# Performance work log

Hardware: AMD Instinct MI355X
Metric: run time of the kernel (lower is better)

The kernel has to match this reference:

```python
import jax, jax.numpy as jnp
import numpy as np

D = 256      # d_model
L = 2        # num_layers
N = 10000    # num_nodes
E = 160000   # num_edges (avg degree 16)
EPS = 1e-5


def _ln(h, g, b):
    m = jnp.mean(h, axis=-1, keepdims=True)
    v = jnp.mean(jnp.square(h - m), axis=-1, keepdims=True)
    return (h - m) / jnp.sqrt(v + EPS) * g + b


def _lrelu(h):
    return jnp.where(h > 0, h, 0.2 * h)


def setup_inputs() -> dict:
    key = jax.random.key(0)
    ks = jax.random.split(key, 24)
    p = lambda k, shape: (jax.random.normal(k, shape, dtype=jnp.float32) * 0.05)
    inp = {
        "edge_index": jax.random.randint(ks[0], (2, E), 0, N),
        "x": jax.random.normal(ks[1], (N, D), dtype=jnp.float32),
        # per-layer attention / FF params (torch Linear convention: W is [out, in])
        "Wq": p(ks[2], (L, D, D)), "bq": p(ks[3], (L, D)),
        "Wk": p(ks[4], (L, D, D)), "bk": p(ks[5], (L, D)),
        "Wv": p(ks[6], (L, D, D)), "bv": p(ks[7], (L, D)),
        "Wff": p(ks[8], (L, D, D)), "bff": p(ks[9], (L, D)),
        # LayerNorm params
        "ga": jnp.ones((L, D), jnp.float32), "ba": jnp.zeros((L, D), jnp.float32),
        "gf": jnp.ones((L, D), jnp.float32), "bf": jnp.zeros((L, D), jnp.float32),
        "gfin": jnp.ones((D,), jnp.float32), "bfin": jnp.zeros((D,), jnp.float32),
        # head MLP
        "W3": p(ks[10], (3 * D, D)), "b3": p(ks[11], (3 * D,)),
        "W4": p(ks[12], (3 * D, 3 * D)), "b4": p(ks[13], (3 * D,)),
        "W5": p(ks[14], (D, 3 * D)), "b5": p(ks[15], (D,)),
        "Wvec": p(ks[16], (1, D)), "bvec": p(ks[17], (1,)),
    }
    return inp


def reference(edge_index, x, Wq, bq, Wk, bk, Wv, bv, Wff, bff,
              ga, ba, gf, bf, gfin, bfin, W3, b3, W4, b4, W5, b5, Wvec, bvec):
    num_nodes = x.shape[0]
    src = edge_index[0]  # [E]
    dst = edge_index[1]  # [E] (segment-softmax target)
    x_i = x[src]         # [E, D]
    query = x[dst]       # [E, D] (x_j)
    for i in range(Wq.shape[0]):
        q = query @ Wq[i].T + bq[i]            # [E, D]
        k = x_i @ Wk[i].T + bk[i]
        v = x_i @ Wv[i].T + bv[i]
        alpha = jnp.sum(q * k, axis=-1)        # [E]
        # segment softmax over dst
        amax = jax.ops.segment_max(alpha, dst, num_segments=num_nodes)
        e = jnp.exp(alpha - amax[dst])
        denom = jax.ops.segment_sum(e, dst, num_segments=num_nodes)
        attn = e / denom[dst]                  # [E]
        attn_out = q + attn[:, None] * v       # [E, D]
        query = _ln(attn_out, ga[i], ba[i])
        query = query @ Wff[i].T + bff[i]
    query = _lrelu(query)
    query = _ln(query, gf[0], bf[0])           # dropout = identity (eval)
    h = _lrelu(query @ W3.T + b3)              # [E, 3D]
    h = _lrelu(h @ W4.T + b4)                  # [E, 3D]
    h = h @ W5.T + b5                          # [E, D]
    h = _ln(h + query, gfin, bfin)
    adj_logits = (h @ Wvec.T + bvec)[:, 0]     # [E]
    return adj_logits
```

## Files before the change

### kernel.cpp

```cpp
#include <hip/hip_runtime.h>

#define D 256

typedef unsigned short u16;
typedef unsigned int u32;
typedef __attribute__((ext_vector_type(8))) short short8;
typedef __attribute__((ext_vector_type(4))) float f32x4;
typedef __attribute__((ext_vector_type(16))) float f32x16;

__device__ __forceinline__ float b2f(u16 u) {
    return __uint_as_float(((u32)u) << 16);
}
__device__ __forceinline__ u16 f2b(float f) {
    u32 u = __float_as_uint(f);
    return (u16)((u + 0x7FFFu + ((u >> 16) & 1u)) >> 16);
}
__device__ __forceinline__ u32 packf(float v) {
    u16 h = f2b(v);
    u16 l = f2b(v - b2f(h));
    return ((u32)h << 16) | l;
}
__device__ __forceinline__ float unpackf(u32 p) {
    return b2f((u16)(p >> 16)) + b2f((u16)(p & 0xffffu));
}
template<typename T> __device__ __forceinline__ float ld1(const T* p);
template<> __device__ __forceinline__ float ld1<u16>(const u16* p) { return b2f(*p); }
template<> __device__ __forceinline__ float ld1<u32>(const u32* p) { return unpackf(*p); }

__device__ __forceinline__ u32 f2ord(float f) {
    u32 b = __float_as_uint(f);
    return (b & 0x80000000u) ? ~b : (b | 0x80000000u);
}
__device__ __forceinline__ float ord2f(u32 u) {
    return (u & 0x80000000u) ? __uint_as_float(u & 0x7fffffffu)
                             : __uint_as_float(~u);
}

__device__ __forceinline__ float wred(float v) {
#pragma unroll
    for (int m = 32; m; m >>= 1) v += __shfl_xor(v, m);
    return v;
}

__device__ __forceinline__ void gl_lds16(const u16* g, u16* l) {
    __builtin_amdgcn_global_load_lds(
        (__attribute__((address_space(1))) void*)(u16*)g,
        (__attribute__((address_space(3))) void*)l, 16, 0, 0);
}

#define VMCNT(n) asm volatile("s_waitcnt vmcnt(" #n ")" ::: "memory")

template<int ACT>
__global__ __launch_bounds__(512, 1)
void gemm2(const u16* __restrict__ A, const u16* __restrict__ Whi,
           const float* __restrict__ bias, u16* __restrict__ C,
           int M, int N, int K)
{
    __shared__ u16 sA[2][128 * 64];
    __shared__ u16 sWh[2][256 * 64];

    const int tid  = threadIdx.x;
    const int lane = tid & 63;
    const int w    = tid >> 6;
    const int wm   = (w & 1) * 64;
    const int wn   = (w >> 1) * 64;
    const int row0 = blockIdx.x * 128;
    const int col0 = blockIdx.y * 256;

    f32x16 acc[2][2];
#pragma unroll
    for (int i = 0; i < 2; ++i)
#pragma unroll
        for (int j = 0; j < 2; ++j)
#pragma unroll
            for (int r = 0; r < 16; ++r) acc[i][j][r] = 0.f;

    const int r31   = lane & 31;
    const int khalf = lane >> 5;
    const int skey  = (r31 & 7) ^ ((r31 >> 3) & 3);
    const int l8r = lane >> 3;
    const int l8c = lane & 7;

    auto STAGE = [&](int b, int k0) {
#pragma unroll
        for (int s = 0; s < 4; ++s) {
            const int rbase = w * 32 + s * 8;
            const int row = rbase + l8r;
            const int gch = l8c ^ (row & 7) ^ s;
            gl_lds16(Whi + (size_t)(col0 + row) * K + k0 + gch * 8,
                     &sWh[b][rbase * 64]);
        }
#pragma unroll
        for (int s = 0; s < 2; ++s) {
            const int rbase = w * 16 + s * 8;
            const int row = rbase + l8r;
            const int gch = l8c ^ (row & 7) ^ ((w * 2 + s) & 3);
            gl_lds16(A + (size_t)(row0 + row) * K + k0 + gch * 8,
                     &sA[b][rbase * 64]);
        }
    };

    auto COMPUTE = [&](int b) {
#pragma unroll
        for (int w4 = 0; w4 < 4; ++w4) {
            const int slot = ((w4 * 2 + khalf) ^ skey) * 8;
            short8 af[2], wf[2];
#pragma unroll
            for (int i = 0; i < 2; ++i)
                af[i] = *(const short8*)(&sA[b][(wm + i * 32 + r31) * 64 + slot]);
#pragma unroll
            for (int j = 0; j < 2; ++j)
                wf[j] = *(const short8*)(&sWh[b][(wn + j * 32 + r31) * 64 + slot]);
#pragma unroll
            for (int i = 0; i < 2; ++i)
#pragma unroll
                for (int j = 0; j < 2; ++j)
                    acc[i][j] = __builtin_amdgcn_mfma_f32_32x32x16_bf16(af[i], wf[j], acc[i][j], 0, 0, 0);
        }
    };

    const int nt = K >> 6;
    STAGE(0, 0);
    STAGE(1, 64);
    int cur = 0;
    for (int t = 0; t < nt - 1; ++t) {
        VMCNT(6);
        __builtin_amdgcn_s_barrier();
        COMPUTE(cur);
        __builtin_amdgcn_s_barrier();
        if (t + 2 < nt) STAGE(cur, (t + 2) << 6);
        cur ^= 1;
    }
    VMCNT(0);
    __builtin_amdgcn_s_barrier();
    COMPUTE(cur);

#pragma unroll
    for (int j = 0; j < 2; ++j) {
        const int col = col0 + wn + j * 32 + r31;
        const float bb = bias[col];
#pragma unroll
        for (int i = 0; i < 2; ++i) {
            const int rowb = row0 + wm + i * 32 + 4 * khalf;
#pragma unroll
            for (int reg = 0; reg < 16; ++reg) {
                const int row = rowb + (reg & 3) + 8 * (reg >> 2);
                float v = acc[i][j][reg] + bb;
                if (ACT) v = v > 0.f ? v : 0.2f * v;
                C[(size_t)row * N + col] = f2b(v);
            }
        }
    }
}

__global__ __launch_bounds__(512, 4)
void gemm3w(const u32* __restrict__ Ap,
            const u16* __restrict__ Whi, const u16* __restrict__ Wlo,
            const float* __restrict__ bias,
            u32* __restrict__ Cp, u16* __restrict__ Chi,
            int M, int K, int act)
{
    constexpr int N = 256;
    __shared__ u16 sAhi[128 * 32];
    __shared__ u16 sAlo[128 * 32];
    __shared__ u16 sWhi[256 * 32];
    __shared__ u16 sWlo[256 * 32];

    const int tid  = threadIdx.x;
    const int lane = tid & 63;
    const int w    = tid >> 6;
    const int wm   = (w & 1) * 64;
    const int wn   = (w >> 1) * 64;
    const int row0 = blockIdx.x * 128;

    f32x4 acc[4][4];
#pragma unroll
    for (int i = 0; i < 4; ++i)
#pragma unroll
        for (int j = 0; j < 4; ++j) acc[i][j] = (f32x4){0.f, 0.f, 0.f, 0.f};

    const int lrow = lane >> 2;
    const int gck  = (lane & 3) ^ ((lane >> 3) & 3);
    const int r15 = lane & 15;
    const int rck = ((lane >> 4) ^ ((r15 >> 1) & 3)) * 8;

    for (int k0 = 0; k0 < K; k0 += 32) {
#pragma unroll
        for (int s = 0; s < 2; ++s) {
            const int rbase = w * 32 + s * 16;
            const size_t gW = (size_t)(rbase + lrow) * K + k0 + gck * 8;
            gl_lds16(Whi + gW, sWhi + rbase * 32);
            gl_lds16(Wlo + gW, sWlo + rbase * 32);
        }
#pragma unroll
        for (int it = 0; it < 2; ++it) {
            const int u = tid + it * 512;
            const int ar = u >> 3;
            const int pos = u & 7;
            uint4 pk = *(const uint4*)(Ap + (size_t)(row0 + ar) * K + k0 + pos * 4);
            const int slot = (pos >> 1) ^ ((ar >> 1) & 3);
            const int base = ar * 32 + slot * 8 + (pos & 1) * 4;
            ushort4 h4, l4;
            h4.x = (u16)(pk.x >> 16); l4.x = (u16)(pk.x & 0xffffu);
            h4.y = (u16)(pk.y >> 16); l4.y = (u16)(pk.y & 0xffffu);
            h4.z = (u16)(pk.z >> 16); l4.z = (u16)(pk.z & 0xffffu);
            h4.w = (u16)(pk.w >> 16); l4.w = (u16)(pk.w & 0xffffu);
            *(ushort4*)(sAhi + base) = h4;
            *(ushort4*)(sAlo + base) = l4;
        }
        __syncthreads();

        short8 ah[4], al[4], wh[4], wl[4];
#pragma unroll
        for (int i = 0; i < 4; ++i) {
            const int offA = (wm + i * 16 + r15) * 32 + rck;
            ah[i] = *(const short8*)(sAhi + offA);
            al[i] = *(const short8*)(sAlo + offA);
        }
#pragma unroll
        for (int j = 0; j < 4; ++j) {
            const int offW = (wn + j * 16 + r15) * 32 + rck;
            wh[j] = *(const short8*)(sWhi + offW);
            wl[j] = *(const short8*)(sWlo + offW);
        }
#pragma unroll
        for (int i = 0; i < 4; ++i)
#pragma unroll
            for (int j = 0; j < 4; ++j) {
                acc[i][j] = __builtin_amdgcn_mfma_f32_16x16x32_bf16(ah[i], wh[j], acc[i][j], 0, 0, 0);
                acc[i][j] = __builtin_amdgcn_mfma_f32_16x16x32_bf16(ah[i], wl[j], acc[i][j], 0, 0, 0);
                acc[i][j] = __builtin_amdgcn_mfma_f32_16x16x32_bf16(al[i], wh[j], acc[i][j], 0, 0, 0);
            }
        __syncthreads();
    }

#pragma unroll
    for (int j = 0; j < 4; ++j) {
        const int col = wn + j * 16 + r15;
        const float bb = bias[col];
#pragma unroll
        for (int i = 0; i < 4; ++i) {
            const int rowb = row0 + wm + i * 16 + (lane >> 4) * 4;
#pragma unroll
            for (int r = 0; r < 4; ++r) {
                float v = acc[i][j][r] + bb;
                if (act) v = v > 0.f ? v : 0.2f * v;
                const size_t idx = (size_t)(rowb + r) * N + col;
                if (Cp) Cp[idx] = packf(v);
                else    Chi[idx] = f2b(v);
            }
        }
    }
}

__global__ __launch_bounds__(512, 4)
void gemm3n(const u32* __restrict__ Ap,
            const u16* __restrict__ Whi, const u16* __restrict__ Wlo,
            const float* __restrict__ b0, const float* __restrict__ b1,
            const float* __restrict__ b2,
            u32* __restrict__ Cp, int M, int K)
{
    constexpr int N = 256;
    __shared__ u16 sAhi[128 * 32];
    __shared__ u16 sAlo[128 * 32];
    __shared__ u16 sWhi[256 * 32];
    __shared__ u16 sWlo[256 * 32];

    const int tid  = threadIdx.x;
    const int lane = tid & 63;
    const int w    = tid >> 6;
    const int wm   = (w & 1) * 64;
    const int wn   = (w >> 1) * 64;
    const int row0 = blockIdx.x * 128;
    const int y    = blockIdx.y;
    const float* bias = (y == 0) ? b0 : ((y == 1) ? b1 : b2);
    const u16* Wh = Whi + (size_t)y * N * K;
    const u16* Wl = Wlo + (size_t)y * N * K;
    u32* Cy = Cp + (size_t)y * M * N;

    f32x4 acc[4][4];
#pragma unroll
    for (int i = 0; i < 4; ++i)
#pragma unroll
        for (int j = 0; j < 4; ++j) acc[i][j] = (f32x4){0.f, 0.f, 0.f, 0.f};

    const int lrow = lane >> 2;
    const int gck  = (lane & 3) ^ ((lane >> 3) & 3);
    const int r15 = lane & 15;
    const int rck = ((lane >> 4) ^ ((r15 >> 1) & 3)) * 8;

    for (int k0 = 0; k0 < K; k0 += 32) {
#pragma unroll
        for (int s = 0; s < 2; ++s) {
            const int rbase = w * 32 + s * 16;
            const size_t gW = (size_t)(rbase + lrow) * K + k0 + gck * 8;
            gl_lds16(Wh + gW, sWhi + rbase * 32);
            gl_lds16(Wl + gW, sWlo + rbase * 32);
        }
#pragma unroll
        for (int it = 0; it < 2; ++it) {
            const int u = tid + it * 512;
            const int ar = u >> 3;
            const int pos = u & 7;
            int arc = row0 + ar; if (arc >= M) arc = M - 1;
            uint4 pk = *(const uint4*)(Ap + (size_t)arc * K + k0 + pos * 4);
            const int slot = (pos >> 1) ^ ((ar >> 1) & 3);
            const int base = ar * 32 + slot * 8 + (pos & 1) * 4;
            ushort4 h4, l4;
            h4.x = (u16)(pk.x >> 16); l4.x = (u16)(pk.x & 0xffffu);
            h4.y = (u16)(pk.y >> 16); l4.y = (u16)(pk.y & 0xffffu);
            h4.z = (u16)(pk.z >> 16); l4.z = (u16)(pk.z & 0xffffu);
            h4.w = (u16)(pk.w >> 16); l4.w = (u16)(pk.w & 0xffffu);
            *(ushort4*)(sAhi + base) = h4;
            *(ushort4*)(sAlo + base) = l4;
        }
        __syncthreads();

        short8 ah[4], al[4], wh[4], wl[4];
#pragma unroll
        for (int i = 0; i < 4; ++i) {
            const int offA = (wm + i * 16 + r15) * 32 + rck;
            ah[i] = *(const short8*)(sAhi + offA);
            al[i] = *(const short8*)(sAlo + offA);
        }
#pragma unroll
        for (int j = 0; j < 4; ++j) {
            const int offW = (wn + j * 16 + r15) * 32 + rck;
            wh[j] = *(const short8*)(sWhi + offW);
            wl[j] = *(const short8*)(sWlo + offW);
        }
#pragma unroll
        for (int i = 0; i < 4; ++i)
#pragma unroll
            for (int j = 0; j < 4; ++j) {
                acc[i][j] = __builtin_amdgcn_mfma_f32_16x16x32_bf16(ah[i], wh[j], acc[i][j], 0, 0, 0);
                acc[i][j] = __builtin_amdgcn_mfma_f32_16x16x32_bf16(ah[i], wl[j], acc[i][j], 0, 0, 0);
                acc[i][j] = __builtin_amdgcn_mfma_f32_16x16x32_bf16(al[i], wh[j], acc[i][j], 0, 0, 0);
            }
        __syncthreads();
    }

#pragma unroll
    for (int j = 0; j < 4; ++j) {
        const int col = wn + j * 16 + r15;
        const float bb = bias[col];
#pragma unroll
        for (int i = 0; i < 4; ++i) {
            const int rowb = row0 + wm + i * 16 + (lane >> 4) * 4;
#pragma unroll
            for (int r = 0; r < 4; ++r) {
                const int row = rowb + r;
                if (row < M)
                    Cy[(size_t)row * N + col] = packf(acc[i][j][r] + bb);
            }
        }
    }
}

__global__ void pack_x(const float* __restrict__ x, u32* __restrict__ xp, int n)
{
    int i = blockIdx.x * 256 + threadIdx.x;
    if (i < n) xp[i] = packf(x[i]);
}

__global__ void wconv(const float* __restrict__ wsrc, u16* __restrict__ hi,
                      u16* __restrict__ lo, int n)
{
    int i = blockIdx.x * 256 + threadIdx.x;
    if (i < n) {
        float v = wsrc[i];
        u16 h = f2b(v);
        hi[i] = h;
        if (lo) lo[i] = f2b(v - b2f(h));
    }
}

__global__ void seg_init(u32* __restrict__ amax, float* __restrict__ denom, int n)
{
    int i = blockIdx.x * 256 + threadIdx.x;
    if (i < n) { amax[i] = 0u; denom[i] = 0.f; }
}

template<typename TQ, int MODE>
__global__ __launch_bounds__(256)
void attn_alpha(const int* __restrict__ src, const int* __restrict__ dst,
                const TQ* __restrict__ qn, const u32* __restrict__ kn,
                float* __restrict__ alpha, u32* __restrict__ amax, int E)
{
    int e = blockIdx.x * 4 + (threadIdx.x >> 6);
    int lane = threadIdx.x & 63;
    if (e >= E) return;
    int s = src[e], d = dst[e];
    const TQ* qp = MODE ? (qn + (size_t)e * D) : (qn + (size_t)d * D);
    const u32* kp = kn + (size_t)s * D;
    float dot = 0.f;
#pragma unroll
    for (int j = 0; j < 4; ++j)
        dot += ld1(qp + lane * 4 + j) * unpackf(kp[lane * 4 + j]);
    dot = wred(dot);
    if (lane == 0) {
        alpha[e] = dot;
        atomicMax(amax + d, f2ord(dot));
    }
}

__global__ void seg_exp(const int* __restrict__ dst, const float* __restrict__ alpha,
                        const u32* __restrict__ amax, float* __restrict__ ebuf,
                        float* __restrict__ denom, int E)
{
    int e = blockIdx.x * 256 + threadIdx.x;
    if (e >= E) return;
    int d = dst[e];
    float ex = expf(alpha[e] - ord2f(amax[d]));
    ebuf[e] = ex;
    atomicAdd(denom + d, ex);
}

template<typename TQ, int MODE>
__global__ __launch_bounds__(256)
void attn_out_ln(const int* __restrict__ src, const int* __restrict__ dst,
                 const TQ* __restrict__ qn, const u32* __restrict__ vn,
                 const float* __restrict__ ebuf, const float* __restrict__ denom,
                 const float* __restrict__ g, const float* __restrict__ bb,
                 u32* __restrict__ outp, int e0, int cm)
{
    int le = blockIdx.x * 4 + (threadIdx.x >> 6);
    int lane = threadIdx.x & 63;
    if (le >= cm) return;
    int ge = e0 + le;
    int s = src[ge], d = dst[ge];
    float attn = ebuf[ge] / denom[d];
    const TQ* qp = MODE ? (qn + (size_t)ge * D) : (qn + (size_t)d * D);
    const u32* vp = vn + (size_t)s * D;
    int d0 = lane * 4;
    float a0 = ld1(qp + d0 + 0) + attn * unpackf(vp[d0 + 0]);
    float a1 = ld1(qp + d0 + 1) + attn * unpackf(vp[d0 + 1]);
    float a2 = ld1(qp + d0 + 2) + attn * unpackf(vp[d0 + 2]);
    float a3 = ld1(qp + d0 + 3) + attn * unpackf(vp[d0 + 3]);
    float mean = wred(a0 + a1 + a2 + a3) * (1.f / D);
    float c0 = a0 - mean, c1 = a1 - mean, c2 = a2 - mean, c3 = a3 - mean;
    float var = wred(c0 * c0 + c1 * c1 + c2 * c2 + c3 * c3) * (1.f / D);
    float rstd = rsqrtf(var + 1e-5f);
    uint4 p;
    p.x = packf(c0 * rstd * g[d0 + 0] + bb[d0 + 0]);
    p.y = packf(c1 * rstd * g[d0 + 1] + bb[d0 + 1]);
    p.z = packf(c2 * rstd * g[d0 + 2] + bb[d0 + 2]);
    p.w = packf(c3 * rstd * g[d0 + 3] + bb[d0 + 3]);
    *(uint4*)(outp + (size_t)le * D + d0) = p;
}

__global__ __launch_bounds__(256)
void lrelu_ln(const u32* __restrict__ inp, const float* __restrict__ g,
              const float* __restrict__ bb, u16* __restrict__ out, int cm)
{
    int le = blockIdx.x * 4 + (threadIdx.x >> 6);
    int lane = threadIdx.x & 63;
    if (le >= cm) return;
    size_t base = (size_t)le * D + lane * 4;
    uint4 xp = *(const uint4*)(inp + base);
    float x0 = unpackf(xp.x), x1 = unpackf(xp.y);
    float x2 = unpackf(xp.z), x3 = unpackf(xp.w);
    float a0 = x0 > 0.f ? x0 : 0.2f * x0;
    float a1 = x1 > 0.f ? x1 : 0.2f * x1;
    float a2 = x2 > 0.f ? x2 : 0.2f * x2;
    float a3 = x3 > 0.f ? x3 : 0.2f * x3;
    float mean = wred(a0 + a1 + a2 + a3) * (1.f / D);
    float c0 = a0 - mean, c1 = a1 - mean, c2 = a2 - mean, c3 = a3 - mean;
    float var = wred(c0 * c0 + c1 * c1 + c2 * c2 + c3 * c3) * (1.f / D);
    float rstd = rsqrtf(var + 1e-5f);
    int d0 = lane * 4;
    ushort4 o;
    o.x = f2b(c0 * rstd * g[d0 + 0] + bb[d0 + 0]);
    o.y = f2b(c1 * rstd * g[d0 + 1] + bb[d0 + 1]);
    o.z = f2b(c2 * rstd * g[d0 + 2] + bb[d0 + 2]);
    o.w = f2b(c3 * rstd * g[d0 + 3] + bb[d0 + 3]);
    *(ushort4*)(out + base) = o;
}

__global__ __launch_bounds__(256)
void final_k(const u16* __restrict__ hp, const u16* __restrict__ qp,
             const float* __restrict__ gfin, const float* __restrict__ bfin,
             const float* __restrict__ wvec, const float* __restrict__ bvec,
             float* __restrict__ out, int e0, int cm)
{
    int le = blockIdx.x * 4 + (threadIdx.x >> 6);
    int lane = threadIdx.x & 63;
    if (le >= cm) return;
    size_t base = (size_t)le * D + lane * 4;
    ushort4 hv = *(const ushort4*)(hp + base);
    ushort4 qv = *(const ushort4*)(qp + base);
    float a0 = b2f(hv.x) + b2f(qv.x);
    float a1 = b2f(hv.y) + b2f(qv.y);
    float a2 = b2f(hv.z) + b2f(qv.z);
    float a3 = b2f(hv.w) + b2f(qv.w);
    float mean = wred(a0 + a1 + a2 + a3) * (1.f / D);
    float c0 = a0 - mean, c1 = a1 - mean, c2 = a2 - mean, c3 = a3 - mean;
    float var = wred(c0 * c0 + c1 * c1 + c2 * c2 + c3 * c3) * (1.f / D);
    float rstd = rsqrtf(var + 1e-5f);
    int d0 = lane * 4;
    float t0 = c0 * rstd * gfin[d0 + 0] + bfin[d0 + 0];
    float t1 = c1 * rstd * gfin[d0 + 1] + bfin[d0 + 1];
    float t2 = c2 * rstd * gfin[d0 + 2] + bfin[d0 + 2];
    float t3 = c3 * rstd * gfin[d0 + 3] + bfin[d0 + 3];
    float part = t0 * wvec[d0 + 0] + t1 * wvec[d0 + 1] +
                 t2 * wvec[d0 + 2] + t3 * wvec[d0 + 3];
    part = wred(part);
    if (lane == 0) out[e0 + le] = part + bvec[0];
}

extern "C" void kernel_launch(void* const* d_in, const int* in_sizes, int n_in,
                              void* d_out, int out_size, void* d_ws, size_t ws_size,
                              hipStream_t stream)
{
    const int*   ei   = (const int*)d_in[0];
    const float* x    = (const float*)d_in[1];
    const float* Wq   = (const float*)d_in[2];
    const float* bq   = (const float*)d_in[3];
    const float* Wk   = (const float*)d_in[4];
    const float* bk   = (const float*)d_in[5];
    const float* Wv   = (const float*)d_in[6];
    const float* bv   = (const float*)d_in[7];
    const float* Wff  = (const float*)d_in[8];
    const float* bff  = (const float*)d_in[9];
    const float* ga   = (const float*)d_in[10];
    const float* ba   = (const float*)d_in[11];
    const float* gf   = (const float*)d_in[12];
    const float* bf   = (const float*)d_in[13];
    const float* gfin = (const float*)d_in[14];
    const float* bfin = (const float*)d_in[15];
    const float* W3   = (const float*)d_in[16];
    const float* b3   = (const float*)d_in[17];
    const float* W4   = (const float*)d_in[18];
    const float* b4   = (const float*)d_in[19];
    const float* W5   = (const float*)d_in[20];
    const float* b5   = (const float*)d_in[21];
    const float* Wvec = (const float*)d_in[22];
    const float* bvec = (const float*)d_in[23];

    const int E  = in_sizes[0] / 2;
    const int Nn = in_sizes[1] / D;
    const int* src = ei;
    const int* dst = ei + E;

    char* base = (char*)d_ws;
    size_t off = 0;
    auto take = [&](size_t bytes) -> void* {
        off = (off + 255) & ~(size_t)255;
        void* r = base + off;
        off += bytes;
        return r;
    };
    u32*   nKV1 = (u32*)take((size_t)2 * Nn * D * 4);
    u16*   q1  = (u16*)take((size_t)E * D * 2);
    float* alpha = (float*)take((size_t)E * 4);
    float* ebuf  = (float*)take((size_t)E * 4);
    u32*   amax  = (u32*)take((size_t)Nn * 4);
    float* denom = (float*)take((size_t)Nn * 4);
    u16* wnh = (u16*)take((size_t)5 * D * D * 2);
    u16* wnl = (u16*)take((size_t)5 * D * D * 2);
    u16* wff0h = (u16*)take((size_t)D * D * 2); u16* wff0l = (u16*)take((size_t)D * D * 2);
    u16* wff1h = (u16*)take((size_t)D * D * 2); u16* wff1l = (u16*)take((size_t)D * D * 2);
    u16* wq1h  = (u16*)take((size_t)D * D * 2); u16* wq1l  = (u16*)take((size_t)D * D * 2);
    u16* w3h = (u16*)take((size_t)3 * D * D * 2);
    u16* w4h = (u16*)take((size_t)9 * D * D * 2);
    u16* w5h = (u16*)take((size_t)3 * D * D * 2);

    const size_t nodeB = (size_t)4 * Nn * D * 4;
    size_t rem = ws_size > off + 8192 ? ws_size - off - 8192 : 0;
    size_t cmA = rem / 4096;
    size_t cmB = rem > nodeB ? (rem - nodeB) / 2048 : 0;
    size_t CMs = (cmA * 2048 >= nodeB) ? cmA : cmB;
    CMs = (CMs / 128) * 128;
    if (CMs > (size_t)E) CMs = E;
    if (CMs > 32768) CMs = 32768;
    if (CMs < 128) CMs = 128;
    const int CM = (int)CMs;

    u32* c1p = (u32*)take((size_t)CM * D * 4);
    u32* c2p = (u32*)take((size_t)CM * D * 4);
    size_t zoneB = (size_t)CM * 2048 > nodeB ? (size_t)CM * 2048 : nodeB;
    char* zone = (char*)take(zoneB);
    u16* c2n = (u16*)zone;
    u16* c3  = (u16*)(zone + (size_t)CM * D * 2);
    u32* xp   = (u32*)zone;
    u32* zQKV = xp + (size_t)Nn * D;
    u32* zQ0 = zQKV;
    u32* zK0 = zQKV + (size_t)Nn * D;
    u32* zV0 = zQKV + (size_t)2 * Nn * D;
    u32* nK1 = nKV1;
    u32* nV1 = nKV1 + (size_t)Nn * D;
    u16* c4 = (u16*)c1p;
    u16* c5 = (u16*)((char*)c1p + (size_t)CM * 3 * D * 2);

    dim3 blk(256);
    dim3 blk2(512);
    int gridSeg = (Nn + 255) / 256;
    int gridE4  = (E + 3) / 4;
    int gridE   = (E + 255) / 256;
    const int DD = D * D;

    pack_x<<<(Nn * D + 255) / 256, 256, 0, stream>>>(x, xp, Nn * D);
    wconv<<<(DD + 255) / 256, 256, 0, stream>>>(Wq,          wnh + 0 * DD, wnl + 0 * DD, DD);
    wconv<<<(DD + 255) / 256, 256, 0, stream>>>(Wk,          wnh + 1 * DD, wnl + 1 * DD, DD);
    wconv<<<(DD + 255) / 256, 256, 0, stream>>>(Wv,          wnh + 2 * DD, wnl + 2 * DD, DD);
    wconv<<<(DD + 255) / 256, 256, 0, stream>>>(Wk + DD,     wnh + 3 * DD, wnl + 3 * DD, DD);
    wconv<<<(DD + 255) / 256, 256, 0, stream>>>(Wv + DD,     wnh + 4 * DD, wnl + 4 * DD, DD);
    wconv<<<(DD + 255) / 256, 256, 0, stream>>>(Wff,         wff0h, wff0l, DD);
    wconv<<<(DD + 255) / 256, 256, 0, stream>>>(Wff + DD,    wff1h, wff1l, DD);
    wconv<<<(DD + 255) / 256, 256, 0, stream>>>(Wq + DD,     wq1h,  wq1l,  DD);
    wconv<<<(3 * DD + 255) / 256, 256, 0, stream>>>(W3, w3h, (u16*)nullptr, 3 * DD);
    wconv<<<(9 * DD + 255) / 256, 256, 0, stream>>>(W4, w4h, (u16*)nullptr, 9 * DD);
    wconv<<<(3 * DD + 255) / 256, 256, 0, stream>>>(W5, w5h, (u16*)nullptr, 3 * DD);

    int gN = (Nn + 127) / 128;
    gemm3n<<<dim3(gN, 3), blk2, 0, stream>>>(xp, wnh, wnl, bq, bk, bv,
                                             zQKV, Nn, D);
    gemm3n<<<dim3(gN, 2), blk2, 0, stream>>>(xp, wnh + 3 * DD, wnl + 3 * DD,
                                             bk + D, bv + D, bv,
                                             nKV1, Nn, D);

    seg_init<<<gridSeg, 256, 0, stream>>>(amax, denom, Nn);
    attn_alpha<u32, 0><<<gridE4, blk, 0, stream>>>(src, dst, zQ0, zK0, alpha, amax, E);
    seg_exp<<<gridE, 256, 0, stream>>>(dst, alpha, amax, ebuf, denom, E);

    for (int e0 = 0; e0 < E; e0 += CM) {
        int cm = E - e0 < CM ? E - e0 : CM;
        int gE4 = (cm + 3) / 4;
        dim3 gD3(cm / 128);
        attn_out_ln<u32, 0><<<gE4, blk, 0, stream>>>(src, dst, zQ0, zV0, ebuf, denom,
                                                     ga, ba, c1p, e0, cm);
        gemm3w<<<gD3, blk2, 0, stream>>>(c1p, wff0h, wff0l, bff,
                                         c2p, (u16*)nullptr, cm, D, 0);
        gemm3w<<<gD3, blk2, 0, stream>>>(c2p, wq1h, wq1l, bq + D,
                                         (u32*)nullptr, q1 + (size_t)e0 * D,
                                         cm, D, 0);
    }

    seg_init<<<gridSeg, 256, 0, stream>>>(amax, denom, Nn);
    attn_alpha<u16, 1><<<gridE4, blk, 0, stream>>>(src, dst, q1, nK1, alpha, amax, E);
    seg_exp<<<gridE, 256, 0, stream>>>(dst, alpha, amax, ebuf, denom, E);

    for (int e0 = 0; e0 < E; e0 += CM) {
        int cm = E - e0 < CM ? E - e0 : CM;
        int gE4 = (cm + 3) / 4;
        dim3 gD3(cm / 128);
        dim3 g2a(cm / 128, (3 * D) / 256);
        dim3 g2b(cm / 128, D / 256);
        attn_out_ln<u16, 1><<<gE4, blk, 0, stream>>>(src, dst, q1, nV1, ebuf, denom,
                                                     ga + D, ba + D, c1p, e0, cm);
        gemm3w<<<gD3, blk2, 0, stream>>>(c1p, wff1h, wff1l, bff + D,
                                         c2p, (u16*)nullptr, cm, D, 0);
        lrelu_ln<<<gE4, blk, 0, stream>>>(c2p, gf, bf, c2n, cm);
        gemm2<1><<<g2a, blk2, 0, stream>>>(c2n, w3h, b3, c3, cm, 3 * D, D);
        gemm2<1><<<g2a, blk2, 0, stream>>>(c3, w4h, b4, c4, cm, 3 * D, 3 * D);
        gemm2<0><<<g2b, blk2, 0, stream>>>(c4, w5h, b5, c5, cm, D, 3 * D);
        final_k<<<gE4, blk, 0, stream>>>(c5, c2n, gfin, bfin, Wvec, bvec,
                                         (float*)d_out, e0, cm);
    }
}
```

Measured before the change: 1.410 ms.

## Add 256-row tile GEMM for head MLP and single-buffer the fallback GEMM

Adds gemm2b, a 256x256-tile bf16 MFMA GEMM where each wave computes a 128x64 sub-tile, with double-buffered LDS and s_setprio around the MFMA bursts. It is used for the W3 and W4 head layers when the chunk size is a multiple of 256, and chunk sizing is rounded to 256 so this is the normal case. The goal is more operand reuse per LDS load and fewer blocks. The old gemm2, still used for W5 and as the fallback, is changed to a single LDS buffer with __syncthreads and launch bounds of 4 to raise occupancy, but this drops its load/compute overlap.

```diff
diff --git a/kernel.cpp b/kernel.cpp
--- a/kernel.cpp
+++ b/kernel.cpp
@@ -52,12 +52,111 @@
 
 template<int ACT>
 __global__ __launch_bounds__(512, 1)
+void gemm2b(const u16* __restrict__ A, const u16* __restrict__ Whi,
+            const float* __restrict__ bias, u16* __restrict__ C,
+            int M, int N, int K)
+{
+    __shared__ u16 sA[2][256 * 64];
+    __shared__ u16 sW[2][256 * 64];
+
+    const int tid  = threadIdx.x;
+    const int lane = tid & 63;
+    const int w    = tid >> 6;
+    const int wm   = (w & 1) * 128;
+    const int wn   = (w >> 1) * 64;
+    const int row0 = blockIdx.x * 256;
+    const int col0 = blockIdx.y * 256;
+
+    f32x16 acc[4][2];
+#pragma unroll
+    for (int i = 0; i < 4; ++i)
+#pragma unroll
+        for (int j = 0; j < 2; ++j)
+#pragma unroll
+            for (int r = 0; r < 16; ++r) acc[i][j][r] = 0.f;
+
+    const int r31   = lane & 31;
+    const int khalf = lane >> 5;
+    const int skey  = (r31 & 7) ^ ((r31 >> 3) & 3);
+    const int l8r = lane >> 3;
+    const int l8c = lane & 7;
+
+    auto STAGE = [&](int b, int k0) {
+#pragma unroll
+        for (int s = 0; s < 4; ++s) {
+            const int rbase = w * 32 + s * 8;
+            const int row = rbase + l8r;
+            const int gch = l8c ^ (row & 7) ^ s;
+            gl_lds16(Whi + (size_t)(col0 + row) * K + k0 + gch * 8,
+                     &sW[b][rbase * 64]);
+            gl_lds16(A + (size_t)(row0 + row) * K + k0 + gch * 8,
+                     &sA[b][rbase * 64]);
+        }
+    };
+
+    auto COMPUTE = [&](int b) {
+#pragma unroll
+        for (int p = 0; p < 4; ++p) {
+            const int slot = ((p * 2 + khalf) ^ skey) * 8;
+            short8 af[4], wf[2];
+#pragma unroll
+            for (int i = 0; i < 4; ++i)
+                af[i] = *(const short8*)(&sA[b][(wm + i * 32 + r31) * 64 + slot]);
+#pragma unroll
+            for (int j = 0; j < 2; ++j)
+                wf[j] = *(const short8*)(&sW[b][(wn + j * 32 + r31) * 64 + slot]);
+            __builtin_amdgcn_s_setprio(1);
+#pragma unroll
+            for (int i = 0; i < 4; ++i)
+#pragma unroll
+                for (int j = 0; j < 2; ++j)
+                    acc[i][j] = __builtin_amdgcn_mfma_f32_32x32x16_bf16(af[i], wf[j], acc[i][j], 0, 0, 0);
+            __builtin_amdgcn_s_setprio(0);
+        }
+    };
+
+    const int nt = K >> 6;
+    STAGE(0, 0);
+    STAGE(1, 64);
+    int cur = 0;
+    for (int t = 0; t < nt - 1; ++t) {
+        VMCNT(8);
+        __builtin_amdgcn_s_barrier();
+        COMPUTE(cur);
+        __builtin_amdgcn_s_barrier();
+        if (t + 2 < nt) STAGE(cur, (t + 2) << 6);
+        cur ^= 1;
+    }
+    VMCNT(0);
+    __builtin_amdgcn_s_barrier();
+    COMPUTE(cur);
+
+#pragma unroll
+    for (int j = 0; j < 2; ++j) {
+        const int col = col0 + wn + j * 32 + r31;
+        const float bb = bias[col];
+#pragma unroll
+        for (int i = 0; i < 4; ++i) {
+            const int rowb = row0 + wm + i * 32 + 4 * khalf;
+#pragma unroll
+            for (int reg = 0; reg < 16; ++reg) {
+                const int row = rowb + (reg & 3) + 8 * (reg >> 2);
+                float v = acc[i][j][reg] + bb;
+                if (ACT) v = v > 0.f ? v : 0.2f * v;
+                C[(size_t)row * N + col] = f2b(v);
+            }
+        }
+    }
+}
+
+template<int ACT>
+__global__ __launch_bounds__(512, 4)
 void gemm2(const u16* __restrict__ A, const u16* __restrict__ Whi,
            const float* __restrict__ bias, u16* __restrict__ C,
            int M, int N, int K)
 {
-    __shared__ u16 sA[2][128 * 64];
-    __shared__ u16 sWh[2][256 * 64];
+    __shared__ u16 sA[128 * 64];
+    __shared__ u16 sWh[256 * 64];
 
     const int tid  = threadIdx.x;
     const int lane = tid & 63;
@@ -81,59 +180,43 @@
     const int l8r = lane >> 3;
     const int l8c = lane & 7;
 
-    auto STAGE = [&](int b, int k0) {
+    for (int k0 = 0; k0 < K; k0 += 64) {
 #pragma unroll
         for (int s = 0; s < 4; ++s) {
             const int rbase = w * 32 + s * 8;
             const int row = rbase + l8r;
             const int gch = l8c ^ (row & 7) ^ s;
-            gl_lds16(Whi + (size_t)(col0 + row) * K + k0 + gch * 8,
-                     &sWh[b][rbase * 64]);
+            const size_t gW = (size_t)(col0 + row) * K + k0 + gch * 8;
+            gl_lds16(Whi + gW, sWh + rbase * 64);
         }
 #pragma unroll
         for (int s = 0; s < 2; ++s) {
             const int rbase = w * 16 + s * 8;
             const int row = rbase + l8r;
             const int gch = l8c ^ (row & 7) ^ ((w * 2 + s) & 3);
-            gl_lds16(A + (size_t)(row0 + row) * K + k0 + gch * 8,
-                     &sA[b][rbase * 64]);
-        }
-    };
-
-    auto COMPUTE = [&](int b) {
+            const size_t gA = (size_t)(row0 + row) * K + k0 + gch * 8;
+            gl_lds16(A + gA, sA + rbase * 64);
+        }
+        __syncthreads();
+
 #pragma unroll
         for (int w4 = 0; w4 < 4; ++w4) {
             const int slot = ((w4 * 2 + khalf) ^ skey) * 8;
             short8 af[2], wf[2];
 #pragma unroll
             for (int i = 0; i < 2; ++i)
-                af[i] = *(const short8*)(&sA[b][(wm + i * 32 + r31) * 64 + slot]);
+                af[i] = *(const short8*)(sA + (wm + i * 32 + r31) * 64 + slot);
 #pragma unroll
             for (int j = 0; j < 2; ++j)
-                wf[j] = *(const short8*)(&sWh[b][(wn + j * 32 + r31) * 64 + slot]);
+                wf[j] = *(const short8*)(sWh + (wn + j * 32 + r31) * 64 + slot);
 #pragma unroll
             for (int i = 0; i < 2; ++i)
 #pragma unroll
                 for (int j = 0; j < 2; ++j)
                     acc[i][j] = __builtin_amdgcn_mfma_f32_32x32x16_bf16(af[i], wf[j], acc[i][j], 0, 0, 0);
         }
-    };
-
-    const int nt = K >> 6;
-    STAGE(0, 0);
-    STAGE(1, 64);
-    int cur = 0;
-    for (int t = 0; t < nt - 1; ++t) {
-        VMCNT(6);
-        __builtin_amdgcn_s_barrier();
-        COMPUTE(cur);
-        __builtin_amdgcn_s_barrier();
-        if (t + 2 < nt) STAGE(cur, (t + 2) << 6);
-        cur ^= 1;
-    }
-    VMCNT(0);
-    __builtin_amdgcn_s_barrier();
-    COMPUTE(cur);
+        __syncthreads();
+    }
 
 #pragma unroll
     for (int j = 0; j < 2; ++j) {
@@ -570,10 +653,10 @@
     size_t cmA = rem / 4096;
     size_t cmB = rem > nodeB ? (rem - nodeB) / 2048 : 0;
     size_t CMs = (cmA * 2048 >= nodeB) ? cmA : cmB;
-    CMs = (CMs / 128) * 128;
+    CMs = (CMs / 256) * 256;
     if (CMs > (size_t)E) CMs = E;
     if (CMs > 32768) CMs = 32768;
-    if (CMs < 128) CMs = 128;
+    if (CMs < 256) CMs = 256;
     const int CM = (int)CMs;
 
     u32* c1p = (u32*)take((size_t)CM * D * 4);
@@ -644,15 +727,21 @@
         int cm = E - e0 < CM ? E - e0 : CM;
         int gE4 = (cm + 3) / 4;
         dim3 gD3(cm / 128);
-        dim3 g2a(cm / 128, (3 * D) / 256);
-        dim3 g2b(cm / 128, D / 256);
         attn_out_ln<u16, 1><<<gE4, blk, 0, stream>>>(src, dst, q1, nV1, ebuf, denom,
                                                      ga + D, ba + D, c1p, e0, cm);
         gemm3w<<<gD3, blk2, 0, stream>>>(c1p, wff1h, wff1l, bff + D,
                                          c2p, (u16*)nullptr, cm, D, 0);
         lrelu_ln<<<gE4, blk, 0, stream>>>(c2p, gf, bf, c2n, cm);
-        gemm2<1><<<g2a, blk2, 0, stream>>>(c2n, w3h, b3, c3, cm, 3 * D, D);
-        gemm2<1><<<g2a, blk2, 0, stream>>>(c3, w4h, b4, c4, cm, 3 * D, 3 * D);
+        if ((cm & 255) == 0) {
+            dim3 gB(cm / 256, (3 * D) / 256);
+            gemm2b<1><<<gB, blk2, 0, stream>>>(c2n, w3h, b3, c3, cm, 3 * D, D);
+            gemm2b<1><<<gB, blk2, 0, stream>>>(c3, w4h, b4, c4, cm, 3 * D, 3 * D);
+        } else {
+            dim3 g2a(cm / 128, (3 * D) / 256);
+            gemm2<1><<<g2a, blk2, 0, stream>>>(c2n, w3h, b3, c3, cm, 3 * D, D);
+            gemm2<1><<<g2a, blk2, 0, stream>>>(c3, w4h, b4, c4, cm, 3 * D, 3 * D);
+        }
+        dim3 g2b(cm / 128, D / 256);
         gemm2<0><<<g2b, blk2, 0, stream>>>(c4, w5h, b5, c5, cm, D, 3 * D);
         final_k<<<gE4, blk, 0, stream>>>(c5, c2n, gfin, bfin, Wvec, bvec,
                                          (float*)d_out, e0, cm);
```

After: 1.457 ms. 3.4% more time.
